# Optimization experiments

Measured on AMD Instinct MI355X. Metric: run time of the kernel, lower is better.

The kernel has to match this reference:

```python
import jax, jax.numpy as jnp
import numpy as np
from jax.ops import segment_sum, segment_max

N = 50000        # nodes
E = 800000       # edges (before self loops)
IN_DIM = 128
HID = 16         # per-head out channels
HEADS = 4
NL = 3           # num GAT layers
OUT = 1
NG = 128         # number of graphs in the batch
NEG = 0.2        # LeakyReLU negative slope (PyG GATConv default)
EPS = 1e-5       # BatchNorm eps


def setup_inputs() -> dict:
    key = jax.random.key(0)
    ks = iter(jax.random.split(key, 64))
    inp = {}
    inp['x'] = jax.random.normal(next(ks), (N, IN_DIM), jnp.float32)
    inp['edge_index'] = jax.random.randint(next(ks), (2, E), 0, N, dtype=jnp.int32)
    inp['batch'] = jnp.sort(jax.random.randint(next(ks), (N,), 0, NG, dtype=jnp.int32))
    d = IN_DIM
    for l in range(NL):
        s = 1.0 / np.sqrt(d)
        inp[f'W{l}'] = jax.random.uniform(next(ks), (HEADS * HID, d), jnp.float32, -s, s)
        inp[f'att_src{l}'] = jax.random.normal(next(ks), (HEADS, HID), jnp.float32) * 0.1
        inp[f'att_dst{l}'] = jax.random.normal(next(ks), (HEADS, HID), jnp.float32) * 0.1
        inp[f'bias{l}'] = jnp.zeros((HEADS * HID,), jnp.float32)
        inp[f'gamma{l}'] = jnp.ones((HEADS * HID,), jnp.float32)
        inp[f'beta{l}'] = jnp.zeros((HEADS * HID,), jnp.float32)
        inp[f'mean{l}'] = jax.random.normal(next(ks), (HEADS * HID,), jnp.float32) * 0.1
        inp[f'var{l}'] = jax.random.uniform(next(ks), (HEADS * HID,), jnp.float32, 0.5, 1.5)
        d = HEADS * HID
    s = 1.0 / np.sqrt(d)
    inp['fcW'] = jax.random.uniform(next(ks), (OUT, d), jnp.float32, -s, s)
    inp['fcb'] = jnp.zeros((OUT,), jnp.float32)
    return inp


def gat_layer(x, src, dst, W, att_src, att_dst, bias):
    """PyG GATConv (concat=True). src/dst already include self loops."""
    n = x.shape[0]
    h = (x @ W.T).reshape(n, HEADS, HID)            # [N,H,C]
    a_s = jnp.sum(h * att_src, axis=-1)             # [N,H]
    a_d = jnp.sum(h * att_dst, axis=-1)             # [N,H]
    logits = a_s[src] + a_d[dst]                    # [Etot,H]
    logits = jnp.where(logits > 0, logits, NEG * logits)  # leaky_relu
    # scatter-softmax over destination-node neighborhoods
    m = segment_max(logits, dst, num_segments=n)
    e = jnp.exp(logits - m[dst])
    z = segment_sum(e, dst, num_segments=n)
    alpha = e / z[dst]                              # [Etot,H]
    out = segment_sum(h[src] * alpha[:, :, None], dst, num_segments=n)  # [N,H,C]
    return out.reshape(n, HEADS * HID) + bias, alpha


def reference(x, edge_index, batch,
              W0, att_src0, att_dst0, bias0, gamma0, beta0, mean0, var0,
              W1, att_src1, att_dst1, bias1, gamma1, beta1, mean1, var1,
              W2, att_src2, att_dst2, bias2, gamma2, beta2, mean2, var2,
              fcW, fcb):
    n = x.shape[0]
    loops = jnp.arange(n, dtype=edge_index.dtype)   # add_self_loops=True
    src = jnp.concatenate([edge_index[0], loops])
    dst = jnp.concatenate([edge_index[1], loops])
    params = [
        (W0, att_src0, att_dst0, bias0, gamma0, beta0, mean0, var0),
        (W1, att_src1, att_dst1, bias1, gamma1, beta1, mean1, var1),
        (W2, att_src2, att_dst2, bias2, gamma2, beta2, mean2, var2),
    ]
    h = x
    alpha0 = None
    for l, (W, a_s, a_d, b, g, be, mu, var) in enumerate(params):
        h, alpha = gat_layer(h, src, dst, W, a_s, a_d, b)
        if l == 0:
            alpha0 = alpha
        h = jax.nn.relu(h)
        h = g * (h - mu) / jnp.sqrt(var + EPS) + be  # BatchNorm1d (eval); dropout = identity
    # global_mean_pool over graph ids
    sums = segment_sum(h, batch, num_segments=NG)
    cnt = segment_sum(jnp.ones((n, 1), h.dtype), batch, num_segments=NG)
    pooled = sums / jnp.maximum(cnt, 1.0)
    out = jax.nn.sigmoid(pooled @ fcW.T + fcb)      # [NG, OUT]
    return out, alpha0
```

## Files before the change

### kernel.cpp

```cpp
#include <hip/hip_runtime.h>
#include <hip/hip_fp16.h>
#include <math.h>

#define NN     50000
#define EE     800000
#define ETOT   (EE + NN)
#define INDIM  128
#define HEADS  4
#define NG     128
#define NEGS   0.2f
#define BNEPS  1e-5f

typedef _Float16 half8 __attribute__((ext_vector_type(8)));
typedef _Float16 half2v __attribute__((ext_vector_type(2)));
typedef float floatx4 __attribute__((ext_vector_type(4)));


__global__ void degree_kernel(const int* __restrict__ ei, int* __restrict__ deg,
                              int* __restrict__ rank) {
    int e = blockIdx.x * blockDim.x + threadIdx.x;
    if (e >= ETOT) return;
    int d = (e < EE) ? ei[EE + e] : (e - EE);
    rank[e] = atomicAdd(&deg[d], 1);
}

__global__ void scan_block_kernel(const int* __restrict__ deg, int* __restrict__ rowstart,
                                  int* __restrict__ bsums) {
    __shared__ int tmp[1024];
    int tid = threadIdx.x;
    int i = blockIdx.x * 1024 + tid;
    int v = (i < NN) ? deg[i] : 0;
    tmp[tid] = v;
    __syncthreads();
    for (int off = 1; off < 1024; off <<= 1) {
        int t = (tid >= off) ? tmp[tid - off] : 0;
        __syncthreads();
        tmp[tid] += t;
        __syncthreads();
    }
    if (i < NN) rowstart[i] = tmp[tid] - v;
    if (tid == 1023) bsums[blockIdx.x] = tmp[tid];
}

__global__ void scan_sums_kernel(int* __restrict__ bsums, int nb) {
    if (threadIdx.x == 0 && blockIdx.x == 0) {
        int acc = 0;
        for (int i = 0; i < nb; ++i) { int t = bsums[i]; bsums[i] = acc; acc += t; }
    }
}

__global__ void add_offsets_kernel(int* __restrict__ rowstart, const int* __restrict__ bsums) {
    int i = blockIdx.x * blockDim.x + threadIdx.x;
    if (i < NN) rowstart[i] += bsums[i >> 10];
}

__global__ void scatter_kernel(const int* __restrict__ ei, const int* __restrict__ rowstart,
                               const int* __restrict__ rank, int4* __restrict__ csr) {
    int e = blockIdx.x * blockDim.x + threadIdx.x;
    if (e >= ETOT) return;
    int s, d;
    if (e < EE) { s = ei[e]; d = ei[EE + e]; }
    else        { s = e - EE; d = e - EE; }
    int pos = rowstart[d] + rank[e];
    csr[pos] = make_int4(s, d, e, 0);
}

__global__ __launch_bounds__(256) void zero_kernel(int* __restrict__ deg,
                                                   float* __restrict__ psums,
                                                   int* __restrict__ pcnt) {
    int i = blockIdx.x * blockDim.x + threadIdx.x;
    if (i < NN) deg[i] = 0;
    else if (i < NN + NG * 64) psums[i - NN] = 0.f;
    else if (i < NN + NG * 64 + NG) pcnt[i - NN - NG * 64] = 0;
}

#define NX8 (NN * INDIM / 8)
__global__ __launch_bounds__(256) void cvt_kernel(const float* __restrict__ x,
                                                  const float* __restrict__ W0,
                                                  const float* __restrict__ W1,
                                                  const float* __restrict__ W2,
                                                  _Float16* __restrict__ Xh,
                                                  _Float16* __restrict__ Wh) {
    int i = blockIdx.x * blockDim.x + threadIdx.x;
    if (i < NX8) {
        float4 v0 = *(const float4*)(x + (size_t)i * 8);
        float4 v1 = *(const float4*)(x + (size_t)i * 8 + 4);
        half8 o;
        o[0] = (_Float16)v0.x; o[1] = (_Float16)v0.y;
        o[2] = (_Float16)v0.z; o[3] = (_Float16)v0.w;
        o[4] = (_Float16)v1.x; o[5] = (_Float16)v1.y;
        o[6] = (_Float16)v1.z; o[7] = (_Float16)v1.w;
        *(half8*)(Xh + (size_t)i * 8) = o;
    } else if (i < NX8 + 2048) {
        int wi = (i - NX8) * 8;
#pragma unroll
        for (int j = 0; j < 8; ++j) {
            int idx = wi + j;
            float v = (idx < 8192) ? W0[idx]
                    : ((idx < 12288) ? W1[idx - 8192] : W2[idx - 12288]);
            Wh[idx] = (_Float16)v;
        }
    }
}

template <int DD>
__global__ __launch_bounds__(256) void gemm_att_kernel(
    const _Float16* __restrict__ X, const _Float16* __restrict__ Wh,
    const float* __restrict__ attS, const float* __restrict__ attD,
    _Float16* __restrict__ H, float* __restrict__ AS, float* __restrict__ AD) {
    constexpr int KB = DD / 32;
    int tid = threadIdx.x;
    int wv = tid >> 6;
    int lane = tid & 63;
    int quad = lane >> 4;
    int n = lane & 15;
    int wbase = blockIdx.x * 64 + wv * 16;

    int arow = wbase + n;
    if (arow >= NN) arow = NN - 1;
    half8 a[KB];
#pragma unroll
    for (int kb = 0; kb < KB; ++kb)
        a[kb] = *(const half8*)(X + (size_t)arow * DD + kb * 32 + quad * 8);

    floatx4 c[4];
#pragma unroll
    for (int t = 0; t < 4; ++t) {
        floatx4 acc = {0.f, 0.f, 0.f, 0.f};
#pragma unroll
        for (int kb = 0; kb < KB; ++kb) {
            half8 b = *(const half8*)(Wh + (size_t)(t * 16 + n) * DD + kb * 32 + quad * 8);
            acc = __builtin_amdgcn_mfma_f32_16x16x32_f16(a[kb], b, acc, 0, 0, 0);
        }
        c[t] = acc;
    }

    float as_l[4], ad_l[4];
#pragma unroll
    for (int t = 0; t < 4; ++t) {
        as_l[t] = attS[t * 16 + n];
        ad_l[t] = attD[t * 16 + n];
    }
#pragma unroll
    for (int r = 0; r < 4; ++r) {
        int node = wbase + quad * 4 + r;
        bool ok = node < NN;
#pragma unroll
        for (int t = 0; t < 4; ++t) {
            float h = c[t][r];
            if (ok) H[(size_t)node * 64 + t * 16 + n] = (_Float16)h;
            float vs = h * as_l[t];
            float vd = h * ad_l[t];
#pragma unroll
            for (int off = 8; off; off >>= 1) {
                vs += __shfl_down(vs, off, 16);
                vd += __shfl_down(vd, off, 16);
            }
            if (ok && n == 0) {
                AS[node * 4 + t] = vs;
                AD[node * 4 + t] = vd;
            }
        }
    }
}

template <bool WRITE_Z>
__global__ __launch_bounds__(256) void edge_aggr_kernel(
    const _Float16* __restrict__ H, const float* __restrict__ AS,
    const float* __restrict__ AD,
    const int* __restrict__ rowstart, const int* __restrict__ deg,
    const int4* __restrict__ csr,
    const float* __restrict__ bias, const float* __restrict__ gamma,
    const float* __restrict__ beta, const float* __restrict__ mean,
    const float* __restrict__ var, _Float16* __restrict__ Hout,
    float* __restrict__ Z) {
    int v = (blockIdx.x * blockDim.x + threadIdx.x) >> 6;
    if (v >= NN) return;
    int lane = threadIdx.x & 63;
    int half = lane >> 5;
    int l32 = lane & 31;
    int head = l32 >> 3;
    int ch2 = l32 * 2;
    float adv = AD[v * 4 + head];
    int start = rowstart[v];
    int cnt = deg[v];
    const int4* srow = csr + start;
    float z = 0.f, acc0 = 0.f, acc1 = 0.f;
    int k = 0;
    for (; k + 8 <= cnt; k += 8) {
        int s0 = srow[k + 0 + half].x;
        int s1 = srow[k + 2 + half].x;
        int s2 = srow[k + 4 + half].x;
        int s3 = srow[k + 6 + half].x;
        float a0 = AS[(size_t)s0 * 4 + head];
        float a1 = AS[(size_t)s1 * 4 + head];
        float a2 = AS[(size_t)s2 * 4 + head];
        float a3 = AS[(size_t)s3 * 4 + head];
        half2v h0 = *(const half2v*)(H + (size_t)s0 * 64 + ch2);
        half2v h1 = *(const half2v*)(H + (size_t)s1 * 64 + ch2);
        half2v h2 = *(const half2v*)(H + (size_t)s2 * 64 + ch2);
        half2v h3 = *(const half2v*)(H + (size_t)s3 * 64 + ch2);
        float l0 = a0 + adv; l0 = l0 > 0.f ? l0 : NEGS * l0; float p0 = __expf(l0);
        float l1 = a1 + adv; l1 = l1 > 0.f ? l1 : NEGS * l1; float p1 = __expf(l1);
        float l2 = a2 + adv; l2 = l2 > 0.f ? l2 : NEGS * l2; float p2 = __expf(l2);
        float l3 = a3 + adv; l3 = l3 > 0.f ? l3 : NEGS * l3; float p3 = __expf(l3);
        z += (p0 + p1) + (p2 + p3);
        acc0 = fmaf(p0, (float)h0[0], acc0); acc1 = fmaf(p0, (float)h0[1], acc1);
        acc0 = fmaf(p1, (float)h1[0], acc0); acc1 = fmaf(p1, (float)h1[1], acc1);
        acc0 = fmaf(p2, (float)h2[0], acc0); acc1 = fmaf(p2, (float)h2[1], acc1);
        acc0 = fmaf(p3, (float)h3[0], acc0); acc1 = fmaf(p3, (float)h3[1], acc1);
    }
    for (; k < cnt; k += 2) {
        int idx = k + half;
        if (idx < cnt) {
            int s = srow[idx].x;
            float a = AS[(size_t)s * 4 + head];
            half2v hv = *(const half2v*)(H + (size_t)s * 64 + ch2);
            float l = a + adv; l = l > 0.f ? l : NEGS * l;
            float p = __expf(l);
            z += p;
            acc0 = fmaf(p, (float)hv[0], acc0);
            acc1 = fmaf(p, (float)hv[1], acc1);
        }
    }
    z    += __shfl_xor(z, 32);
    acc0 += __shfl_xor(acc0, 32);
    acc1 += __shfl_xor(acc1, 32);
    if (half == 0) {
        if (WRITE_Z && (l32 & 7) == 0) Z[v * 4 + head] = z;
        float2 bi = *(const float2*)(bias + ch2);
        float2 ga = *(const float2*)(gamma + ch2);
        float2 be = *(const float2*)(beta + ch2);
        float2 mu = *(const float2*)(mean + ch2);
        float2 va = *(const float2*)(var + ch2);
        float r0 = fmaxf(acc0 / z + bi.x, 0.f);
        float r1 = fmaxf(acc1 / z + bi.y, 0.f);
        r0 = ga.x * (r0 - mu.x) * rsqrtf(va.x + BNEPS) + be.x;
        r1 = ga.y * (r1 - mu.y) * rsqrtf(va.y + BNEPS) + be.y;
        half2v o;
        o[0] = (_Float16)r0;
        o[1] = (_Float16)r1;
        *(half2v*)(Hout + (size_t)v * 64 + ch2) = o;
    }
}

__global__ __launch_bounds__(256) void alpha_kernel(
    const float* __restrict__ AS, const float* __restrict__ AD,
    const float* __restrict__ Z, const int4* __restrict__ csr,
    float* __restrict__ alpha_out) {
    int j = blockIdx.x * blockDim.x + threadIdx.x;
    if (j >= ETOT) return;
    int4 en = csr[j];
    float4 as = *(const float4*)(AS + (size_t)en.x * 4);
    float4 ad = *(const float4*)(AD + (size_t)en.y * 4);
    float4 z4 = *(const float4*)(Z + (size_t)en.y * 4);
    float l;
    float4 a;
    l = as.x + ad.x; l = l > 0.f ? l : NEGS * l; a.x = __expf(l) / z4.x;
    l = as.y + ad.y; l = l > 0.f ? l : NEGS * l; a.y = __expf(l) / z4.y;
    l = as.z + ad.z; l = l > 0.f ? l : NEGS * l; a.z = __expf(l) / z4.z;
    l = as.w + ad.w; l = l > 0.f ? l : NEGS * l; a.w = __expf(l) / z4.w;
    *(float4*)(alpha_out + (size_t)en.z * 4) = a;
}

__global__ __launch_bounds__(256) void pool_kernel(const __half* __restrict__ H,
                                                   const int* __restrict__ batch,
                                                   float* __restrict__ sums,
                                                   int* __restrict__ cnt) {
    int wid = (blockIdx.x * blockDim.x + threadIdx.x) >> 6;
    int lane = threadIdx.x & 63;
    int base = wid * 64;
    if (base >= NN) return;
    int end = min(base + 64, NN);
    int cur = batch[base];
    float acc = 0.f;
    int c0 = 0;
    for (int i = base; i < end; ++i) {
        int g = batch[i];
        if (g != cur) {
            atomicAdd(&sums[cur * 64 + lane], acc);
            if (lane == 0) atomicAdd(&cnt[cur], c0);
            cur = g; acc = 0.f; c0 = 0;
        }
        acc += __half2float(H[(size_t)i * 64 + lane]);
        c0++;
    }
    atomicAdd(&sums[cur * 64 + lane], acc);
    if (lane == 0) atomicAdd(&cnt[cur], c0);
}

__global__ void fc_kernel(const float* __restrict__ sums, const int* __restrict__ cnt,
                          const float* __restrict__ fcW, const float* __restrict__ fcb,
                          float* __restrict__ out) {
    int g = (blockIdx.x * blockDim.x + threadIdx.x) >> 6;
    int lane = threadIdx.x & 63;
    if (g >= NG) return;
    float c = fmaxf((float)cnt[g], 1.f);
    float val = (sums[g * 64 + lane] / c) * fcW[lane];
#pragma unroll
    for (int off = 32; off; off >>= 1) val += __shfl_down(val, off, 64);
    if (lane == 0) out[g] = 1.f / (1.f + expf(-(val + fcb[0])));
}

extern "C" void kernel_launch(void* const* d_in, const int* in_sizes, int n_in,
                              void* d_out, int out_size, void* d_ws, size_t ws_size,
                              hipStream_t stream) {
    const float* x   = (const float*)d_in[0];
    const int* ei    = (const int*)d_in[1];
    const int* batch = (const int*)d_in[2];
    const float* W[3], *attS[3], *attD[3], *bias[3], *gamma[3], *beta[3], *mean[3], *var[3];
    for (int l = 0; l < 3; ++l) {
        W[l]     = (const float*)d_in[3 + 8 * l + 0];
        attS[l]  = (const float*)d_in[3 + 8 * l + 1];
        attD[l]  = (const float*)d_in[3 + 8 * l + 2];
        bias[l]  = (const float*)d_in[3 + 8 * l + 3];
        gamma[l] = (const float*)d_in[3 + 8 * l + 4];
        beta[l]  = (const float*)d_in[3 + 8 * l + 5];
        mean[l]  = (const float*)d_in[3 + 8 * l + 6];
        var[l]   = (const float*)d_in[3 + 8 * l + 7];
    }
    const float* fcW = (const float*)d_in[27];
    const float* fcb = (const float*)d_in[28];
    float* out = (float*)d_out;
    float* alpha_out = (float*)d_out + NG;

    char* p = (char*)d_ws;
    auto carve = [&](size_t bytes) {
        char* q = p;
        p += (bytes + 255) & ~(size_t)255;
        return q;
    };
    _Float16* Xh    = (_Float16*)carve(sizeof(_Float16) * NN * INDIM);
    _Float16* Wh    = (_Float16*)carve(sizeof(_Float16) * 16384);
    _Float16* Hh    = (_Float16*)carve(sizeof(_Float16) * NN * 64);
    _Float16* Hn    = (_Float16*)carve(sizeof(_Float16) * NN * 64);
    float* AS       = (float*)carve(sizeof(float) * NN * 4);
    float* AD       = (float*)carve(sizeof(float) * NN * 4);
    float* Z        = (float*)carve(sizeof(float) * NN * 4);
    int*   rowstart = (int*)carve(sizeof(int) * NN);
    int*   deg      = (int*)carve(sizeof(int) * NN);
    int*   rank     = (int*)carve(sizeof(int) * ETOT);
    int*   bsums    = (int*)carve(sizeof(int) * 64);
    int4*  csr      = (int4*)carve(sizeof(int4) * ETOT);
    float* psums    = (float*)carve(sizeof(float) * NG * 64);
    int*   pcnt     = (int*)carve(sizeof(int) * NG);

    zero_kernel<<<(NN + NG * 64 + NG + 255) / 256, 256, 0, stream>>>(deg, psums, pcnt);

    cvt_kernel<<<(NX8 + 2048 + 255) / 256, 256, 0, stream>>>(x, W[0], W[1], W[2], Xh, Wh);

    int nbScan = (NN + 1023) / 1024;
    degree_kernel<<<(ETOT + 255) / 256, 256, 0, stream>>>(ei, deg, rank);
    scan_block_kernel<<<nbScan, 1024, 0, stream>>>(deg, rowstart, bsums);
    scan_sums_kernel<<<1, 64, 0, stream>>>(bsums, nbScan);
    add_offsets_kernel<<<(NN + 255) / 256, 256, 0, stream>>>(rowstart, bsums);
    scatter_kernel<<<(ETOT + 255) / 256, 256, 0, stream>>>(ei, rowstart, rank, csr);

    int edgeBlocks = (NN * 64 + 255) / 256;
    int posBlocks = (ETOT + 255) / 256;
    int gemmBlocks = (NN + 63) / 64;

    gemm_att_kernel<128><<<gemmBlocks, 256, 0, stream>>>(Xh, Wh, attS[0], attD[0],
                                                         Hh, AS, AD);
    edge_aggr_kernel<true><<<edgeBlocks, 256, 0, stream>>>(
        Hh, AS, AD, rowstart, deg, csr,
        bias[0], gamma[0], beta[0], mean[0], var[0], Hn, Z);
    alpha_kernel<<<posBlocks, 256, 0, stream>>>(AS, AD, Z, csr, alpha_out);

    gemm_att_kernel<64><<<gemmBlocks, 256, 0, stream>>>(Hn, Wh + 8192, attS[1], attD[1],
                                                        Hh, AS, AD);
    edge_aggr_kernel<false><<<edgeBlocks, 256, 0, stream>>>(
        Hh, AS, AD, rowstart, deg, csr,
        bias[1], gamma[1], beta[1], mean[1], var[1], Hn, nullptr);

    gemm_att_kernel<64><<<gemmBlocks, 256, 0, stream>>>(Hn, Wh + 12288, attS[2], attD[2],
                                                        Hh, AS, AD);
    edge_aggr_kernel<false><<<edgeBlocks, 256, 0, stream>>>(
        Hh, AS, AD, rowstart, deg, csr,
        bias[2], gamma[2], beta[2], mean[2], var[2], Hn, nullptr);

    int poolWaves = (NN + 63) / 64;
    pool_kernel<<<(poolWaves * 64 + 255) / 256, 256, 0, stream>>>(
        (const __half*)Hn, batch, psums, pcnt);
    fc_kernel<<<(NG * 64 + 255) / 256, 256, 0, stream>>>(psums, pcnt, fcW, fcb, out);
}
```

Before: 380.1 us.

## Shrink CSR to source-only ints, read alpha edges directly, fuse zero and convert kernels

The CSR array now stores only the source index (4 bytes) instead of an int4 of source, destination, edge id and padding (16 bytes), which cuts scatter writes and the CSR reads in all three edge aggregation passes. The alpha kernel now walks edges in original order straight from edge_index, so it no longer needs the destination or edge id from the CSR and writes coalesced output. Each half-wave now reads four consecutive entries instead of interleaved ones. The zero-init and fp16 conversion kernels are merged into one launch to save a kernel launch.

```diff
diff --git a/kernel.cpp b/kernel.cpp
--- a/kernel.cpp
+++ b/kernel.cpp
@@ -55,32 +55,27 @@
 }
 
 __global__ void scatter_kernel(const int* __restrict__ ei, const int* __restrict__ rowstart,
-                               const int* __restrict__ rank, int4* __restrict__ csr) {
+                               const int* __restrict__ rank, int* __restrict__ csr) {
     int e = blockIdx.x * blockDim.x + threadIdx.x;
     if (e >= ETOT) return;
     int s, d;
     if (e < EE) { s = ei[e]; d = ei[EE + e]; }
     else        { s = e - EE; d = e - EE; }
     int pos = rowstart[d] + rank[e];
-    csr[pos] = make_int4(s, d, e, 0);
-}
-
-__global__ __launch_bounds__(256) void zero_kernel(int* __restrict__ deg,
+    csr[pos] = s;
+}
+
+#define NX8 (NN * INDIM / 8)
+#define PREP_TOT (NX8 + 2048 + NN + NG * 64 + NG)
+__global__ __launch_bounds__(256) void prep_kernel(const float* __restrict__ x,
+                                                   const float* __restrict__ W0,
+                                                   const float* __restrict__ W1,
+                                                   const float* __restrict__ W2,
+                                                   _Float16* __restrict__ Xh,
+                                                   _Float16* __restrict__ Wh,
+                                                   int* __restrict__ deg,
                                                    float* __restrict__ psums,
                                                    int* __restrict__ pcnt) {
-    int i = blockIdx.x * blockDim.x + threadIdx.x;
-    if (i < NN) deg[i] = 0;
-    else if (i < NN + NG * 64) psums[i - NN] = 0.f;
-    else if (i < NN + NG * 64 + NG) pcnt[i - NN - NG * 64] = 0;
-}
-
-#define NX8 (NN * INDIM / 8)
-__global__ __launch_bounds__(256) void cvt_kernel(const float* __restrict__ x,
-                                                  const float* __restrict__ W0,
-                                                  const float* __restrict__ W1,
-                                                  const float* __restrict__ W2,
-                                                  _Float16* __restrict__ Xh,
-                                                  _Float16* __restrict__ Wh) {
     int i = blockIdx.x * blockDim.x + threadIdx.x;
     if (i < NX8) {
         float4 v0 = *(const float4*)(x + (size_t)i * 8);
@@ -100,6 +95,12 @@
                     : ((idx < 12288) ? W1[idx - 8192] : W2[idx - 12288]);
             Wh[idx] = (_Float16)v;
         }
+    } else if (i < NX8 + 2048 + NN) {
+        deg[i - NX8 - 2048] = 0;
+    } else if (i < NX8 + 2048 + NN + NG * 64) {
+        psums[i - NX8 - 2048 - NN] = 0.f;
+    } else if (i < PREP_TOT) {
+        pcnt[i - NX8 - 2048 - NN - NG * 64] = 0;
     }
 }
 
@@ -169,7 +170,7 @@
     const _Float16* __restrict__ H, const float* __restrict__ AS,
     const float* __restrict__ AD,
     const int* __restrict__ rowstart, const int* __restrict__ deg,
-    const int4* __restrict__ csr,
+    const int* __restrict__ csr,
     const float* __restrict__ bias, const float* __restrict__ gamma,
     const float* __restrict__ beta, const float* __restrict__ mean,
     const float* __restrict__ var, _Float16* __restrict__ Hout,
@@ -184,14 +185,15 @@
     float adv = AD[v * 4 + head];
     int start = rowstart[v];
     int cnt = deg[v];
-    const int4* srow = csr + start;
+    const int* srow = csr + start;
     float z = 0.f, acc0 = 0.f, acc1 = 0.f;
     int k = 0;
     for (; k + 8 <= cnt; k += 8) {
-        int s0 = srow[k + 0 + half].x;
-        int s1 = srow[k + 2 + half].x;
-        int s2 = srow[k + 4 + half].x;
-        int s3 = srow[k + 6 + half].x;
+        int b = k + half * 4;
+        int s0 = srow[b + 0];
+        int s1 = srow[b + 1];
+        int s2 = srow[b + 2];
+        int s3 = srow[b + 3];
         float a0 = AS[(size_t)s0 * 4 + head];
         float a1 = AS[(size_t)s1 * 4 + head];
         float a2 = AS[(size_t)s2 * 4 + head];
@@ -213,7 +215,7 @@
     for (; k < cnt; k += 2) {
         int idx = k + half;
         if (idx < cnt) {
-            int s = srow[idx].x;
+            int s = srow[idx];
             float a = AS[(size_t)s * 4 + head];
             half2v hv = *(const half2v*)(H + (size_t)s * 64 + ch2);
             float l = a + adv; l = l > 0.f ? l : NEGS * l;
@@ -245,22 +247,24 @@
 }
 
 __global__ __launch_bounds__(256) void alpha_kernel(
+    const int* __restrict__ ei,
     const float* __restrict__ AS, const float* __restrict__ AD,
-    const float* __restrict__ Z, const int4* __restrict__ csr,
-    float* __restrict__ alpha_out) {
-    int j = blockIdx.x * blockDim.x + threadIdx.x;
-    if (j >= ETOT) return;
-    int4 en = csr[j];
-    float4 as = *(const float4*)(AS + (size_t)en.x * 4);
-    float4 ad = *(const float4*)(AD + (size_t)en.y * 4);
-    float4 z4 = *(const float4*)(Z + (size_t)en.y * 4);
+    const float* __restrict__ Z, float* __restrict__ alpha_out) {
+    int e = blockIdx.x * blockDim.x + threadIdx.x;
+    if (e >= ETOT) return;
+    int s, d;
+    if (e < EE) { s = ei[e]; d = ei[EE + e]; }
+    else        { s = e - EE; d = e - EE; }
+    float4 as = *(const float4*)(AS + (size_t)s * 4);
+    float4 ad = *(const float4*)(AD + (size_t)d * 4);
+    float4 z4 = *(const float4*)(Z + (size_t)d * 4);
     float l;
     float4 a;
     l = as.x + ad.x; l = l > 0.f ? l : NEGS * l; a.x = __expf(l) / z4.x;
     l = as.y + ad.y; l = l > 0.f ? l : NEGS * l; a.y = __expf(l) / z4.y;
     l = as.z + ad.z; l = l > 0.f ? l : NEGS * l; a.z = __expf(l) / z4.z;
     l = as.w + ad.w; l = l > 0.f ? l : NEGS * l; a.w = __expf(l) / z4.w;
-    *(float4*)(alpha_out + (size_t)en.z * 4) = a;
+    *(float4*)(alpha_out + (size_t)e * 4) = a;
 }
 
 __global__ __launch_bounds__(256) void pool_kernel(const __half* __restrict__ H,
@@ -341,13 +345,12 @@
     int*   deg      = (int*)carve(sizeof(int) * NN);
     int*   rank     = (int*)carve(sizeof(int) * ETOT);
     int*   bsums    = (int*)carve(sizeof(int) * 64);
-    int4*  csr      = (int4*)carve(sizeof(int4) * ETOT);
+    int*   csr      = (int*)carve(sizeof(int) * ETOT);
     float* psums    = (float*)carve(sizeof(float) * NG * 64);
     int*   pcnt     = (int*)carve(sizeof(int) * NG);
 
-    zero_kernel<<<(NN + NG * 64 + NG + 255) / 256, 256, 0, stream>>>(deg, psums, pcnt);
-
-    cvt_kernel<<<(NX8 + 2048 + 255) / 256, 256, 0, stream>>>(x, W[0], W[1], W[2], Xh, Wh);
+    prep_kernel<<<(PREP_TOT + 255) / 256, 256, 0, stream>>>(
+        x, W[0], W[1], W[2], Xh, Wh, deg, psums, pcnt);
 
     int nbScan = (NN + 1023) / 1024;
     degree_kernel<<<(ETOT + 255) / 256, 256, 0, stream>>>(ei, deg, rank);
@@ -365,7 +368,7 @@
     edge_aggr_kernel<true><<<edgeBlocks, 256, 0, stream>>>(
         Hh, AS, AD, rowstart, deg, csr,
         bias[0], gamma[0], beta[0], mean[0], var[0], Hn, Z);
-    alpha_kernel<<<posBlocks, 256, 0, stream>>>(AS, AD, Z, csr, alpha_out);
+    alpha_kernel<<<posBlocks, 256, 0, stream>>>(ei, AS, AD, Z, alpha_out);
 
     gemm_att_kernel<64><<<gemmBlocks, 256, 0, stream>>>(Hn, Wh + 8192, attS[1], attD[1],
                                                         Hh, AS, AD);
```

Measured after the change: 377.1 us. No clear change (-0.8%).
